# Kernel optimization log

Hardware: AMD Instinct MI355X
Metric: run time of the kernel (lower is better)

Reference implementation:

```python
import jax, jax.numpy as jnp
import numpy as np

L, D, H, N, B, R = 6, 1024, 16, 2048, 1, 10000
K = D // H
EPS = 1e-6


def setup_inputs() -> dict:
    key = jax.random.key(0)
    ks = jax.random.split(key, 7)
    s = 0.02
    return {
        "x": jax.random.normal(ks[0], (B, N, D), dtype=jnp.float32),
        "qkv_w": jax.random.normal(ks[1], (L, 3 * D, D), dtype=jnp.float32) * s,
        "out_w": jax.random.normal(ks[2], (L, D, D), dtype=jnp.float32) * s,
        "w1": jax.random.normal(ks[3], (L, 8 * D, D), dtype=jnp.float32) * s,
        "w2": jax.random.normal(ks[4], (L, D, 4 * D), dtype=jnp.float32) * s,
        "norm1_w": jnp.ones((L, D), dtype=jnp.float32),
        "norm2_w": jnp.ones((L, D), dtype=jnp.float32),
    }


def _rmsnorm(x, w):
    var = jnp.mean(jnp.square(x), axis=-1, keepdims=True)
    return x * jax.lax.rsqrt(var + EPS) * w


def _rope_tables():
    inv_freq = 1.0 / (R ** (jnp.arange(0, K, 2, dtype=jnp.float32) / K))
    t = jnp.arange(N, dtype=jnp.float32)
    freqs = jnp.outer(t, inv_freq)            # (N, K/2)
    emb = jnp.concatenate([freqs, freqs], -1)  # (N, K)
    # broadcast over (B, N, H, K)
    return jnp.cos(emb)[None, :, None, :], jnp.sin(emb)[None, :, None, :]


def _rotate_half(x):
    x1, x2 = jnp.split(x, 2, axis=-1)
    return jnp.concatenate([-x2, x1], axis=-1)


def _apply_rope(q, k, cos, sin):
    return q * cos + _rotate_half(q) * sin, k * cos + _rotate_half(k) * sin


def reference(x, qkv_w, out_w, w1, w2, norm1_w, norm2_w):
    cos, sin = _rope_tables()
    causal = jnp.tril(jnp.ones((N, N), dtype=bool))  # (N_query, M_key)
    scale = 1.0 / jnp.sqrt(jnp.float32(K))
    for i in range(L):
        # --- attention block (pre-norm) ---
        h = _rmsnorm(x, norm1_w[i])
        qkv = jnp.einsum('bnd,ed->bne', h, qkv_w[i]).reshape(B, N, 3, H, K)
        q, k, v = qkv[:, :, 0], qkv[:, :, 1], qkv[:, :, 2]
        q, k = _apply_rope(q, k, cos, sin)
        scores = jnp.einsum('bnhk,bmhk->bnhm', q, k) * scale
        scores = jnp.where(causal[None, :, None, :], scores, -jnp.inf)
        probs = jax.nn.softmax(scores, axis=-1)
        attn = jnp.einsum('bnhm,bmhk->bnhk', probs, v).reshape(B, N, D)
        x = x + jnp.einsum('bnd,ed->bne', attn, out_w[i])
        # --- SwiGLU MLP block (pre-norm) ---
        h = _rmsnorm(x, norm2_w[i])
        a = jnp.einsum('bnd,ed->bne', h, w1[i])  # (B, N, 8D)
        a1, a2 = jnp.split(a, 2, axis=-1)
        g = jax.nn.silu(a1) * a2                 # (B, N, 4D)
        x = x + jnp.einsum('bnf,df->bnd', g, w2[i])
    return x
```

## Files before the change

kernel.cpp:

```cpp
#include <hip/hip_runtime.h>
#include <math.h>

typedef short bf16x8 __attribute__((ext_vector_type(8)));
typedef float floatx4 __attribute__((ext_vector_type(4)));

__device__ __forceinline__ unsigned short f2bf(float f) {
    unsigned int u = __float_as_uint(f);
    u += 0x7fffu + ((u >> 16) & 1u);
    return (unsigned short)(u >> 16);
}
__device__ __forceinline__ float bf2f(unsigned short u) {
    return __uint_as_float(((unsigned int)u) << 16);
}
__device__ __forceinline__ void async16(void* lds, const void* g) {
    __builtin_amdgcn_global_load_lds((const __attribute__((address_space(1))) unsigned int*)g,
                                     (__attribute__((address_space(3))) unsigned int*)lds,
                                     16, 0, 0);
}

__global__ __launch_bounds__(256) void conv_w(
        const float* __restrict__ qkv, const float* __restrict__ ow,
        const float* __restrict__ w1, const float* __restrict__ w2,
        unsigned short* __restrict__ dst) {
    size_t i = (size_t)blockIdx.x * 256 + threadIdx.x;
    const float* s; size_t off; unsigned short* d;
    if (i < 786432)       { s = qkv; off = i;           d = dst; }
    else if (i < 1048576) { s = ow;  off = i - 786432;  d = dst + 3145728; }
    else if (i < 3145728) { s = w1;  off = i - 1048576; d = dst + 4194304; }
    else                  { s = w2;  off = i - 3145728; d = dst + 12582912; }
    float4 v = ((const float4*)s)[off];
    ushort4 o;
    o.x = f2bf(v.x); o.y = f2bf(v.y); o.z = f2bf(v.z); o.w = f2bf(v.w);
    ((ushort4*)d)[off] = o;
}

__global__ __launch_bounds__(256) void rmsnorm_bf(
        const float* __restrict__ x, const float* __restrict__ w,
        unsigned short* __restrict__ out) {
    __shared__ float sred[4];
    int row = blockIdx.x;
    int t = threadIdx.x;
    float4 v = ((const float4*)(x + (size_t)row * 1024))[t];
    float ss = v.x*v.x + v.y*v.y + v.z*v.z + v.w*v.w;
#pragma unroll
    for (int m = 32; m >= 1; m >>= 1) ss += __shfl_xor(ss, m, 64);
    if ((t & 63) == 0) sred[t >> 6] = ss;
    __syncthreads();
    float tot = sred[0] + sred[1] + sred[2] + sred[3];
    float r = rsqrtf(tot * (1.0f / 1024.0f) + 1e-6f);
    float4 wv = ((const float4*)w)[t];
    ushort4 o;
    o.x = f2bf(v.x * r * wv.x); o.y = f2bf(v.y * r * wv.y);
    o.z = f2bf(v.z * r * wv.z); o.w = f2bf(v.w * r * wv.w);
    ((ushort4*)(out + (size_t)row * 1024))[t] = o;
}

template<int OUTMODE>
__global__ __launch_bounds__(256) void gemm_bf(
        const unsigned short* __restrict__ A, const unsigned short* __restrict__ W,
        void* __restrict__ Cout, int Ncols, int Kd) {
    __shared__ __align__(16) unsigned short As[128 * 32];
    __shared__ __align__(16) unsigned short Bs[128 * 32];
    int t = threadIdx.x;
    int wave = t >> 6, lane = t & 63;
    int wm = wave >> 1, wn = wave & 1;
    int lrow = lane & 15, quad = lane >> 4;
    int bmBase = blockIdx.y * 128, bnBase = blockIdx.x * 128;
    int kslice = Kd / gridDim.z;
    int kBeg = blockIdx.z * kslice, kEnd = kBeg + kslice;

    int sub = lane >> 2;
    int colb = (lane & 3) * 8;
    int c0 = wave, c1 = wave + 4;

    floatx4 acc[4][4] = {};

    for (int k0 = kBeg; k0 < kEnd; k0 += 32) {
        async16(&As[c0 * 512 + lane * 8], A + (size_t)(bmBase + c0 * 16 + sub) * Kd + k0 + colb);
        async16(&As[c1 * 512 + lane * 8], A + (size_t)(bmBase + c1 * 16 + sub) * Kd + k0 + colb);
        async16(&Bs[c0 * 512 + lane * 8], W + (size_t)(bnBase + c0 * 16 + sub) * Kd + k0 + colb);
        async16(&Bs[c1 * 512 + lane * 8], W + (size_t)(bnBase + c1 * 16 + sub) * Kd + k0 + colb);
        __syncthreads();
        bf16x8 af[4], bfr[4];
#pragma unroll
        for (int im = 0; im < 4; im++)
            af[im] = *(const bf16x8*)&As[(wm * 64 + im * 16 + lrow) * 32 + quad * 8];
#pragma unroll
        for (int in = 0; in < 4; in++)
            bfr[in] = *(const bf16x8*)&Bs[(wn * 64 + in * 16 + lrow) * 32 + quad * 8];
#pragma unroll
        for (int im = 0; im < 4; im++)
#pragma unroll
            for (int in = 0; in < 4; in++)
                acc[im][in] = __builtin_amdgcn_mfma_f32_16x16x32_bf16(af[im], bfr[in], acc[im][in], 0, 0, 0);
        __syncthreads();
    }

#pragma unroll
    for (int im = 0; im < 4; im++) {
        int gr0 = bmBase + wm * 64 + im * 16 + quad * 4;
#pragma unroll
        for (int in = 0; in < 4; in++) {
            int gc = bnBase + wn * 64 + in * 16 + lrow;
#pragma unroll
            for (int r2 = 0; r2 < 4; r2++) {
                size_t off = (size_t)(gr0 + r2) * Ncols + gc;
                if (OUTMODE == 0) ((unsigned short*)Cout)[off] = f2bf(acc[im][in][r2]);
                else              atomicAdd((float*)Cout + off, acc[im][in][r2]);
            }
        }
    }
}

__global__ __launch_bounds__(512) void rope_bf(
        const unsigned short* __restrict__ qkv, unsigned short* __restrict__ q,
        unsigned short* __restrict__ k, unsigned short* __restrict__ vt) {
    int n = blockIdx.x;
    int t = threadIdx.x;
    int h = t >> 5, j = t & 31;
    float inv = powf(10000.0f, -(float)j * (1.0f / 32.0f));
    float ang = (float)n * inv;
    float s = sinf(ang), c = cosf(ang);
    const unsigned short* base = qkv + (size_t)n * 3072;
    int o1 = h * 64 + j, o2 = o1 + 32;
    float q1 = bf2f(base[o1]),        q2 = bf2f(base[o2]);
    float k1 = bf2f(base[1024 + o1]), k2 = bf2f(base[1024 + o2]);
    q[(size_t)n * 1024 + o1] = f2bf(q1 * c - q2 * s);
    q[(size_t)n * 1024 + o2] = f2bf(q2 * c + q1 * s);
    k[(size_t)n * 1024 + o1] = f2bf(k1 * c - k2 * s);
    k[(size_t)n * 1024 + o2] = f2bf(k2 * c + k1 * s);
    vt[(size_t)o1 * 2048 + n] = base[2048 + o1];
    vt[(size_t)o2 * 2048 + n] = base[2048 + o2];
}

__global__ __launch_bounds__(256) void attn_bf(
        const unsigned short* __restrict__ q, const unsigned short* __restrict__ kbuf,
        const unsigned short* __restrict__ vt, unsigned short* __restrict__ attn) {
    __shared__ __align__(16) unsigned short Qs[64 * 64];
    __shared__ __align__(16) unsigned short Ks[64 * 64];
    __shared__ __align__(16) unsigned short Vs[64 * 64];
    __shared__ __align__(16) unsigned short Ps[4 * 16 * 64];
    int qb = blockIdx.x;
    int h  = blockIdx.y;
    int t = threadIdx.x;
    int wave = t >> 6, lane = t & 63;
    int lrow = lane & 15, quad = lane >> 4;
    int sub8 = lane >> 3;
    int col8 = (lane & 7) * 8;
    int c0 = wave, c1 = wave + 4;

    async16(&Qs[c0 * 512 + lane * 8], q + (size_t)(qb * 64 + c0 * 8 + sub8) * 1024 + h * 64 + col8);
    async16(&Qs[c1 * 512 + lane * 8], q + (size_t)(qb * 64 + c1 * 8 + sub8) * 1024 + h * 64 + col8);

    floatx4 oacc[4] = {};
    float mrow[4], lsum[4];
#pragma unroll
    for (int r2 = 0; r2 < 4; r2++) { mrow[r2] = -INFINITY; lsum[r2] = 0.0f; }

    for (int kt = 0; kt <= qb; ++kt) {
        __syncthreads();
        async16(&Ks[c0 * 512 + lane * 8], kbuf + (size_t)(kt * 64 + c0 * 8 + sub8) * 1024 + h * 64 + col8);
        async16(&Ks[c1 * 512 + lane * 8], kbuf + (size_t)(kt * 64 + c1 * 8 + sub8) * 1024 + h * 64 + col8);
        async16(&Vs[c0 * 512 + lane * 8], vt + (size_t)(h * 64 + c0 * 8 + sub8) * 2048 + kt * 64 + col8);
        async16(&Vs[c1 * 512 + lane * 8], vt + (size_t)(h * 64 + c1 * 8 + sub8) * 2048 + kt * 64 + col8);
        __syncthreads();

        floatx4 sacc[4] = {};
#pragma unroll
        for (int kk = 0; kk < 64; kk += 32) {
            bf16x8 aq = *(const bf16x8*)&Qs[(wave * 16 + lrow) * 64 + kk + quad * 8];
#pragma unroll
            for (int jn = 0; jn < 4; jn++) {
                bf16x8 bk = *(const bf16x8*)&Ks[(jn * 16 + lrow) * 64 + kk + quad * 8];
                sacc[jn] = __builtin_amdgcn_mfma_f32_16x16x32_bf16(aq, bk, sacc[jn], 0, 0, 0);
            }
        }

#pragma unroll
        for (int r2 = 0; r2 < 4; r2++) {
            int qg = qb * 64 + wave * 16 + quad * 4 + r2;
            float sv[4];
            float rm = -INFINITY;
#pragma unroll
            for (int jn = 0; jn < 4; jn++) {
                float xv = sacc[jn][r2] * 0.125f;
                int kg = kt * 64 + jn * 16 + lrow;
                if (kg > qg) xv = -INFINITY;
                sv[jn] = xv;
                rm = fmaxf(rm, xv);
            }
#pragma unroll
            for (int m = 8; m >= 1; m >>= 1) rm = fmaxf(rm, __shfl_xor(rm, m, 64));
            float mnew = fmaxf(mrow[r2], rm);
            float alpha = __expf(mrow[r2] - mnew);
            float rs = 0.0f;
#pragma unroll
            for (int jn = 0; jn < 4; jn++) {
                float p = __expf(sv[jn] - mnew);
                rs += p;
                Ps[wave * 1024 + (quad * 4 + r2) * 64 + jn * 16 + lrow] = f2bf(p);
            }
#pragma unroll
            for (int m = 8; m >= 1; m >>= 1) rs += __shfl_xor(rs, m, 64);
            lsum[r2] = lsum[r2] * alpha + rs;
            mrow[r2] = mnew;
#pragma unroll
            for (int jd = 0; jd < 4; jd++) oacc[jd][r2] *= alpha;
        }
        __syncthreads();

#pragma unroll
        for (int kk = 0; kk < 64; kk += 32) {
            bf16x8 ap = *(const bf16x8*)&Ps[wave * 1024 + lrow * 64 + kk + quad * 8];
#pragma unroll
            for (int jd = 0; jd < 4; jd++) {
                bf16x8 bv = *(const bf16x8*)&Vs[(jd * 16 + lrow) * 64 + kk + quad * 8];
                oacc[jd] = __builtin_amdgcn_mfma_f32_16x16x32_bf16(ap, bv, oacc[jd], 0, 0, 0);
            }
        }
    }

#pragma unroll
    for (int r2 = 0; r2 < 4; r2++) {
        int qg = qb * 64 + wave * 16 + quad * 4 + r2;
        float invl = 1.0f / lsum[r2];
#pragma unroll
        for (int jd = 0; jd < 4; jd++)
            attn[(size_t)qg * 1024 + h * 64 + jd * 16 + lrow] = f2bf(oacc[jd][r2] * invl);
    }
}

__global__ __launch_bounds__(256) void silu_bf(
        const unsigned short* __restrict__ a, unsigned short* __restrict__ g) {
    int i = blockIdx.x * 256 + threadIdx.x;
    int n = i >> 10, c = (i & 1023) << 2;
    ushort4 a1 = *(const ushort4*)(a + (size_t)n * 8192 + c);
    ushort4 a2 = *(const ushort4*)(a + (size_t)n * 8192 + 4096 + c);
    float x0 = bf2f(a1.x), x1 = bf2f(a1.y), x2 = bf2f(a1.z), x3 = bf2f(a1.w);
    ushort4 o;
    o.x = f2bf(x0 / (1.0f + __expf(-x0)) * bf2f(a2.x));
    o.y = f2bf(x1 / (1.0f + __expf(-x1)) * bf2f(a2.y));
    o.z = f2bf(x2 / (1.0f + __expf(-x2)) * bf2f(a2.z));
    o.w = f2bf(x3 / (1.0f + __expf(-x3)) * bf2f(a2.w));
    *(ushort4*)(g + (size_t)n * 4096 + c) = o;
}

extern "C" void kernel_launch(void* const* d_in, const int* in_sizes, int n_in,
                              void* d_out, int out_size, void* d_ws, size_t ws_size,
                              hipStream_t stream) {
    const float* x     = (const float*)d_in[0];
    const float* qkv_w = (const float*)d_in[1];
    const float* out_w = (const float*)d_in[2];
    const float* w1    = (const float*)d_in[3];
    const float* w2    = (const float*)d_in[4];
    const float* n1    = (const float*)d_in[5];
    const float* n2    = (const float*)d_in[6];

    char* ws = (char*)d_ws;
    float*          xbuf  = (float*)ws;
    unsigned short* hbuf  = (unsigned short*)(ws + 8388608);
    unsigned short* wslot = (unsigned short*)(ws + 12582912);
    char*           arena = ws + 46137344;
    unsigned short* qkvb  = (unsigned short*)arena;
    unsigned short* qb_   = (unsigned short*)(arena + 12582912);
    unsigned short* kb_   = (unsigned short*)(arena + 16777216);
    unsigned short* vtb   = (unsigned short*)(arena + 20971520);
    unsigned short* attnb = (unsigned short*)(arena + 25165824);
    unsigned short* abuf  = (unsigned short*)arena;
    unsigned short* gbuf  = (unsigned short*)(arena + 33554432);

    unsigned short* qkvw_bf = wslot;
    unsigned short* outw_bf = wslot + 3145728;
    unsigned short* w1_bf   = wslot + 4194304;
    unsigned short* w2_bf   = wslot + 12582912;

    hipMemcpyAsync(xbuf, x, (size_t)2048 * 1024 * 4, hipMemcpyDeviceToDevice, stream);

    for (int i = 0; i < 6; i++) {
        conv_w<<<16384, 256, 0, stream>>>(qkv_w + (size_t)i * 3145728, out_w + (size_t)i * 1048576,
                                          w1 + (size_t)i * 8388608, w2 + (size_t)i * 4194304, wslot);
        rmsnorm_bf<<<2048, 256, 0, stream>>>(xbuf, n1 + (size_t)i * 1024, hbuf);
        gemm_bf<0><<<dim3(24, 16, 1), 256, 0, stream>>>(hbuf, qkvw_bf, qkvb, 3072, 1024);
        rope_bf<<<2048, 512, 0, stream>>>(qkvb, qb_, kb_, vtb);
        attn_bf<<<dim3(32, 16), 256, 0, stream>>>(qb_, kb_, vtb, attnb);
        gemm_bf<1><<<dim3(8, 16, 2), 256, 0, stream>>>(attnb, outw_bf, xbuf, 1024, 1024);
        rmsnorm_bf<<<2048, 256, 0, stream>>>(xbuf, n2 + (size_t)i * 1024, hbuf);
        gemm_bf<0><<<dim3(64, 16, 1), 256, 0, stream>>>(hbuf, w1_bf, abuf, 8192, 1024);
        silu_bf<<<8192, 256, 0, stream>>>(abuf, gbuf);
        gemm_bf<1><<<dim3(8, 16, 4), 256, 0, stream>>>(gbuf, w2_bf, xbuf, 1024, 4096);
    }

    hipMemcpyAsync(d_out, xbuf, (size_t)2048 * 1024 * 4, hipMemcpyDeviceToDevice, stream);
}
```

Measured before the change: 2.108 ms.

## Fuse RoPE into QKV GEMM, SiLU into W1 GEMM, batch weight conversion

The QKV GEMM epilogue now applies the rotary embedding directly and writes Q, K and transposed V, which removes the separate rope kernel and the intermediate qkv buffer. The W1 GEMM computes the gate and up tiles together and applies SiLU in its epilogue, so the 8D activation round-trip and the silu kernel go away. All six layers' weights are converted to bf16 in a single launch up front rather than once per layer. The trade-offs are higher register pressure in the dual-accumulator GEMM, half as many blocks for the W1 GEMM, and a larger workspace.

After: 3.470 ms. 64.6% more time.

```diff
diff --git a/kernel.cpp b/kernel.cpp
--- a/kernel.cpp
+++ b/kernel.cpp
@@ -18,20 +18,33 @@
                                      16, 0, 0);
 }
 
-__global__ __launch_bounds__(256) void conv_w(
+__global__ __launch_bounds__(256) void conv_all(
         const float* __restrict__ qkv, const float* __restrict__ ow,
         const float* __restrict__ w1, const float* __restrict__ w2,
         unsigned short* __restrict__ dst) {
     size_t i = (size_t)blockIdx.x * 256 + threadIdx.x;
-    const float* s; size_t off; unsigned short* d;
-    if (i < 786432)       { s = qkv; off = i;           d = dst; }
-    else if (i < 1048576) { s = ow;  off = i - 786432;  d = dst + 3145728; }
-    else if (i < 3145728) { s = w1;  off = i - 1048576; d = dst + 4194304; }
-    else                  { s = w2;  off = i - 3145728; d = dst + 12582912; }
-    float4 v = ((const float4*)s)[off];
+    const float4* s; size_t didx;
+    if (i < 4718592) {
+        size_t layer = i / 786432, off = i % 786432;
+        s = (const float4*)qkv + layer * 786432 + off;
+        didx = layer * 4194304 + off;
+    } else if (i < 6291456) {
+        size_t j = i - 4718592, layer = j / 262144, off = j % 262144;
+        s = (const float4*)ow + layer * 262144 + off;
+        didx = layer * 4194304 + 786432 + off;
+    } else if (i < 18874368) {
+        size_t j = i - 6291456, layer = j / 2097152, off = j % 2097152;
+        s = (const float4*)w1 + layer * 2097152 + off;
+        didx = layer * 4194304 + 1048576 + off;
+    } else {
+        size_t j = i - 18874368, layer = j / 1048576, off = j % 1048576;
+        s = (const float4*)w2 + layer * 1048576 + off;
+        didx = layer * 4194304 + 3145728 + off;
+    }
+    float4 v = *s;
     ushort4 o;
     o.x = f2bf(v.x); o.y = f2bf(v.y); o.z = f2bf(v.z); o.w = f2bf(v.w);
-    ((ushort4*)d)[off] = o;
+    ((ushort4*)dst)[didx] = o;
 }
 
 __global__ __launch_bounds__(256) void rmsnorm_bf(
@@ -55,10 +68,9 @@
     ((ushort4*)(out + (size_t)row * 1024))[t] = o;
 }
 
-template<int OUTMODE>
-__global__ __launch_bounds__(256) void gemm_bf(
+__global__ __launch_bounds__(256) void gemm_atomic(
         const unsigned short* __restrict__ A, const unsigned short* __restrict__ W,
-        void* __restrict__ Cout, int Ncols, int Kd) {
+        float* __restrict__ Cout, int Ncols, int Kd) {
     __shared__ __align__(16) unsigned short As[128 * 32];
     __shared__ __align__(16) unsigned short Bs[128 * 32];
     int t = threadIdx.x;
@@ -68,9 +80,7 @@
     int bmBase = blockIdx.y * 128, bnBase = blockIdx.x * 128;
     int kslice = Kd / gridDim.z;
     int kBeg = blockIdx.z * kslice, kEnd = kBeg + kslice;
-
-    int sub = lane >> 2;
-    int colb = (lane & 3) * 8;
+    int sub = lane >> 2, colb = (lane & 3) * 8;
     int c0 = wave, c1 = wave + 4;
 
     floatx4 acc[4][4] = {};
@@ -103,34 +113,148 @@
         for (int in = 0; in < 4; in++) {
             int gc = bnBase + wn * 64 + in * 16 + lrow;
 #pragma unroll
+            for (int r2 = 0; r2 < 4; r2++)
+                atomicAdd(Cout + (size_t)(gr0 + r2) * Ncols + gc, acc[im][in][r2]);
+        }
+    }
+}
+
+__global__ __launch_bounds__(256) void gemm_qkv(
+        const unsigned short* __restrict__ A, const unsigned short* __restrict__ W,
+        unsigned short* __restrict__ qout, unsigned short* __restrict__ kout,
+        unsigned short* __restrict__ vtout) {
+    __shared__ __align__(16) unsigned short As[128 * 32];
+    __shared__ __align__(16) unsigned short Bs[128 * 32];
+    const int Kd = 1024;
+    int t = threadIdx.x;
+    int wave = t >> 6, lane = t & 63;
+    int wm = wave >> 1, wn = wave & 1;
+    int lrow = lane & 15, quad = lane >> 4;
+    int bmBase = blockIdx.y * 128, bnBase = blockIdx.x * 128;
+    int sub = lane >> 2, colb = (lane & 3) * 8;
+    int c0 = wave, c1 = wave + 4;
+
+    floatx4 acc[4][4] = {};
+
+    for (int k0 = 0; k0 < Kd; k0 += 32) {
+        async16(&As[c0 * 512 + lane * 8], A + (size_t)(bmBase + c0 * 16 + sub) * Kd + k0 + colb);
+        async16(&As[c1 * 512 + lane * 8], A + (size_t)(bmBase + c1 * 16 + sub) * Kd + k0 + colb);
+        async16(&Bs[c0 * 512 + lane * 8], W + (size_t)(bnBase + c0 * 16 + sub) * Kd + k0 + colb);
+        async16(&Bs[c1 * 512 + lane * 8], W + (size_t)(bnBase + c1 * 16 + sub) * Kd + k0 + colb);
+        __syncthreads();
+        bf16x8 af[4], bfr[4];
+#pragma unroll
+        for (int im = 0; im < 4; im++)
+            af[im] = *(const bf16x8*)&As[(wm * 64 + im * 16 + lrow) * 32 + quad * 8];
+#pragma unroll
+        for (int in = 0; in < 4; in++)
+            bfr[in] = *(const bf16x8*)&Bs[(wn * 64 + in * 16 + lrow) * 32 + quad * 8];
+#pragma unroll
+        for (int im = 0; im < 4; im++)
+#pragma unroll
+            for (int in = 0; in < 4; in++)
+                acc[im][in] = __builtin_amdgcn_mfma_f32_16x16x32_bf16(af[im], bfr[in], acc[im][in], 0, 0, 0);
+        __syncthreads();
+    }
+
+    int region = bnBase >> 10;
+    int cb = bnBase & 1023;
+    int headbase = cb + wn * 64;
+    if (region < 2) {
+        unsigned short* dst = (region == 0) ? qout : kout;
+#pragma unroll
+        for (int in = 0; in < 2; in++) {
+            int j = in * 16 + lrow;
+            float invf = exp2f(-(float)j * (13.2877123795494f / 32.0f));
+#pragma unroll
+            for (int im = 0; im < 4; im++) {
+                int n0 = bmBase + wm * 64 + im * 16 + quad * 4;
+#pragma unroll
+                for (int r2 = 0; r2 < 4; r2++) {
+                    int n = n0 + r2;
+                    float ang = (float)n * invf;
+                    float s = sinf(ang), c = cosf(ang);
+                    float x1 = acc[im][in][r2], x2 = acc[im][in + 2][r2];
+                    dst[(size_t)n * 1024 + headbase + j]      = f2bf(x1 * c - x2 * s);
+                    dst[(size_t)n * 1024 + headbase + j + 32] = f2bf(x2 * c + x1 * s);
+                }
+            }
+        }
+    } else {
+#pragma unroll
+        for (int im = 0; im < 4; im++) {
+            int n0 = bmBase + wm * 64 + im * 16 + quad * 4;
+#pragma unroll
+            for (int in = 0; in < 4; in++) {
+                int d = headbase + in * 16 + lrow;
+                ushort4 o;
+                o.x = f2bf(acc[im][in][0]); o.y = f2bf(acc[im][in][1]);
+                o.z = f2bf(acc[im][in][2]); o.w = f2bf(acc[im][in][3]);
+                *(ushort4*)&vtout[(size_t)d * 2048 + n0] = o;
+            }
+        }
+    }
+}
+
+__global__ __launch_bounds__(256) void gemm_w1silu(
+        const unsigned short* __restrict__ A, const unsigned short* __restrict__ W,
+        unsigned short* __restrict__ g) {
+    __shared__ __align__(16) unsigned short As[128 * 32];
+    __shared__ __align__(16) unsigned short Bg[128 * 32];
+    __shared__ __align__(16) unsigned short Bu[128 * 32];
+    const int Kd = 1024;
+    int t = threadIdx.x;
+    int wave = t >> 6, lane = t & 63;
+    int wm = wave >> 1, wn = wave & 1;
+    int lrow = lane & 15, quad = lane >> 4;
+    int bmBase = blockIdx.y * 128, bnBase = blockIdx.x * 128;
+    int sub = lane >> 2, colb = (lane & 3) * 8;
+    int c0 = wave, c1 = wave + 4;
+
+    floatx4 accg[4][4] = {};
+    floatx4 accu[4][4] = {};
+
+    for (int k0 = 0; k0 < Kd; k0 += 32) {
+        async16(&As[c0 * 512 + lane * 8], A + (size_t)(bmBase + c0 * 16 + sub) * Kd + k0 + colb);
+        async16(&As[c1 * 512 + lane * 8], A + (size_t)(bmBase + c1 * 16 + sub) * Kd + k0 + colb);
+        async16(&Bg[c0 * 512 + lane * 8], W + (size_t)(bnBase + c0 * 16 + sub) * Kd + k0 + colb);
+        async16(&Bg[c1 * 512 + lane * 8], W + (size_t)(bnBase + c1 * 16 + sub) * Kd + k0 + colb);
+        async16(&Bu[c0 * 512 + lane * 8], W + (size_t)(4096 + bnBase + c0 * 16 + sub) * Kd + k0 + colb);
+        async16(&Bu[c1 * 512 + lane * 8], W + (size_t)(4096 + bnBase + c1 * 16 + sub) * Kd + k0 + colb);
+        __syncthreads();
+        bf16x8 af[4], bg[4], bu[4];
+#pragma unroll
+        for (int im = 0; im < 4; im++)
+            af[im] = *(const bf16x8*)&As[(wm * 64 + im * 16 + lrow) * 32 + quad * 8];
+#pragma unroll
+        for (int in = 0; in < 4; in++) {
+            bg[in] = *(const bf16x8*)&Bg[(wn * 64 + in * 16 + lrow) * 32 + quad * 8];
+            bu[in] = *(const bf16x8*)&Bu[(wn * 64 + in * 16 + lrow) * 32 + quad * 8];
+        }
+#pragma unroll
+        for (int im = 0; im < 4; im++)
+#pragma unroll
+            for (int in = 0; in < 4; in++) {
+                accg[im][in] = __builtin_amdgcn_mfma_f32_16x16x32_bf16(af[im], bg[in], accg[im][in], 0, 0, 0);
+                accu[im][in] = __builtin_amdgcn_mfma_f32_16x16x32_bf16(af[im], bu[in], accu[im][in], 0, 0, 0);
+            }
+        __syncthreads();
+    }
+
+#pragma unroll
+    for (int im = 0; im < 4; im++) {
+        int gr0 = bmBase + wm * 64 + im * 16 + quad * 4;
+#pragma unroll
+        for (int in = 0; in < 4; in++) {
+            int gc = bnBase + wn * 64 + in * 16 + lrow;
+#pragma unroll
             for (int r2 = 0; r2 < 4; r2++) {
-                size_t off = (size_t)(gr0 + r2) * Ncols + gc;
-                if (OUTMODE == 0) ((unsigned short*)Cout)[off] = f2bf(acc[im][in][r2]);
-                else              atomicAdd((float*)Cout + off, acc[im][in][r2]);
-            }
-        }
-    }
-}
-
-__global__ __launch_bounds__(512) void rope_bf(
-        const unsigned short* __restrict__ qkv, unsigned short* __restrict__ q,
-        unsigned short* __restrict__ k, unsigned short* __restrict__ vt) {
-    int n = blockIdx.x;
-    int t = threadIdx.x;
-    int h = t >> 5, j = t & 31;
-    float inv = powf(10000.0f, -(float)j * (1.0f / 32.0f));
-    float ang = (float)n * inv;
-    float s = sinf(ang), c = cosf(ang);
-    const unsigned short* base = qkv + (size_t)n * 3072;
-    int o1 = h * 64 + j, o2 = o1 + 32;
-    float q1 = bf2f(base[o1]),        q2 = bf2f(base[o2]);
-    float k1 = bf2f(base[1024 + o1]), k2 = bf2f(base[1024 + o2]);
-    q[(size_t)n * 1024 + o1] = f2bf(q1 * c - q2 * s);
-    q[(size_t)n * 1024 + o2] = f2bf(q2 * c + q1 * s);
-    k[(size_t)n * 1024 + o1] = f2bf(k1 * c - k2 * s);
-    k[(size_t)n * 1024 + o2] = f2bf(k2 * c + k1 * s);
-    vt[(size_t)o1 * 2048 + n] = base[2048 + o1];
-    vt[(size_t)o2 * 2048 + n] = base[2048 + o2];
+                float a1 = accg[im][in][r2], a2 = accu[im][in][r2];
+                float gv = a1 / (1.0f + __expf(-a1)) * a2;
+                g[(size_t)(gr0 + r2) * 4096 + gc] = f2bf(gv);
+            }
+        }
+    }
 }
 
 __global__ __launch_bounds__(256) void attn_bf(
@@ -145,8 +269,7 @@
     int t = threadIdx.x;
     int wave = t >> 6, lane = t & 63;
     int lrow = lane & 15, quad = lane >> 4;
-    int sub8 = lane >> 3;
-    int col8 = (lane & 7) * 8;
+    int sub8 = lane >> 3, col8 = (lane & 7) * 8;
     int c0 = wave, c1 = wave + 4;
 
     async16(&Qs[c0 * 512 + lane * 8], q + (size_t)(qb * 64 + c0 * 8 + sub8) * 1024 + h * 64 + col8);
@@ -228,21 +351,6 @@
         for (int jd = 0; jd < 4; jd++)
             attn[(size_t)qg * 1024 + h * 64 + jd * 16 + lrow] = f2bf(oacc[jd][r2] * invl);
     }
-}
-
-__global__ __launch_bounds__(256) void silu_bf(
-        const unsigned short* __restrict__ a, unsigned short* __restrict__ g) {
-    int i = blockIdx.x * 256 + threadIdx.x;
-    int n = i >> 10, c = (i & 1023) << 2;
-    ushort4 a1 = *(const ushort4*)(a + (size_t)n * 8192 + c);
-    ushort4 a2 = *(const ushort4*)(a + (size_t)n * 8192 + 4096 + c);
-    float x0 = bf2f(a1.x), x1 = bf2f(a1.y), x2 = bf2f(a1.z), x3 = bf2f(a1.w);
-    ushort4 o;
-    o.x = f2bf(x0 / (1.0f + __expf(-x0)) * bf2f(a2.x));
-    o.y = f2bf(x1 / (1.0f + __expf(-x1)) * bf2f(a2.y));
-    o.z = f2bf(x2 / (1.0f + __expf(-x2)) * bf2f(a2.z));
-    o.w = f2bf(x3 / (1.0f + __expf(-x3)) * bf2f(a2.w));
-    *(ushort4*)(g + (size_t)n * 4096 + c) = o;
 }
 
 extern "C" void kernel_launch(void* const* d_in, const int* in_sizes, int n_in,
@@ -259,35 +367,30 @@
     char* ws = (char*)d_ws;
     float*          xbuf  = (float*)ws;
     unsigned short* hbuf  = (unsigned short*)(ws + 8388608);
-    unsigned short* wslot = (unsigned short*)(ws + 12582912);
-    char*           arena = ws + 46137344;
-    unsigned short* qkvb  = (unsigned short*)arena;
-    unsigned short* qb_   = (unsigned short*)(arena + 12582912);
-    unsigned short* kb_   = (unsigned short*)(arena + 16777216);
-    unsigned short* vtb   = (unsigned short*)(arena + 20971520);
-    unsigned short* attnb = (unsigned short*)(arena + 25165824);
-    unsigned short* abuf  = (unsigned short*)arena;
-    unsigned short* gbuf  = (unsigned short*)(arena + 33554432);
-
-    unsigned short* qkvw_bf = wslot;
-    unsigned short* outw_bf = wslot + 3145728;
-    unsigned short* w1_bf   = wslot + 4194304;
-    unsigned short* w2_bf   = wslot + 12582912;
+    unsigned short* qb_   = (unsigned short*)(ws + 12582912);
+    unsigned short* kb_   = (unsigned short*)(ws + 16777216);
+    unsigned short* vtb   = (unsigned short*)(ws + 20971520);
+    unsigned short* attnb = (unsigned short*)(ws + 25165824);
+    unsigned short* gbuf  = (unsigned short*)(ws + 29360128);
+    unsigned short* wslot = (unsigned short*)(ws + 46137344);
 
     hipMemcpyAsync(xbuf, x, (size_t)2048 * 1024 * 4, hipMemcpyDeviceToDevice, stream);
+    conv_all<<<98304, 256, 0, stream>>>(qkv_w, out_w, w1, w2, wslot);
 
     for (int i = 0; i < 6; i++) {
-        conv_w<<<16384, 256, 0, stream>>>(qkv_w + (size_t)i * 3145728, out_w + (size_t)i * 1048576,
-                                          w1 + (size_t)i * 8388608, w2 + (size_t)i * 4194304, wslot);
+        unsigned short* wb = wslot + (size_t)i * 16777216;
+        unsigned short* qkvw = wb;
+        unsigned short* outw = wb + 3145728;
+        unsigned short* w1w  = wb + 4194304;
+        unsigned short* w2w  = wb + 12582912;
+
         rmsnorm_bf<<<2048, 256, 0, stream>>>(xbuf, n1 + (size_t)i * 1024, hbuf);
-        gemm_bf<0><<<dim3(24, 16, 1), 256, 0, stream>>>(hbuf, qkvw_bf, qkvb, 3072, 1024);
-        rope_bf<<<2048, 512, 0, stream>>>(qkvb, qb_, kb_, vtb);
+        gemm_qkv<<<dim3(24, 16), 256, 0, stream>>>(hbuf, qkvw, qb_, kb_, vtb);
         attn_bf<<<dim3(32, 16), 256, 0, stream>>>(qb_, kb_, vtb, attnb);
-        gemm_bf<1><<<dim3(8, 16, 2), 256, 0, stream>>>(attnb, outw_bf, xbuf, 1024, 1024);
+        gemm_atomic<<<dim3(8, 16, 2), 256, 0, stream>>>(attnb, outw, xbuf, 1024, 1024);
         rmsnorm_bf<<<2048, 256, 0, stream>>>(xbuf, n2 + (size_t)i * 1024, hbuf);
-        gemm_bf<0><<<dim3(64, 16, 1), 256, 0, stream>>>(hbuf, w1_bf, abuf, 8192, 1024);
-        silu_bf<<<8192, 256, 0, stream>>>(abuf, gbuf);
-        gemm_bf<1><<<dim3(8, 16, 4), 256, 0, stream>>>(gbuf, w2_bf, xbuf, 1024, 4096);
+        gemm_w1silu<<<dim3(32, 16), 256, 0, stream>>>(hbuf, w1w, gbuf);
+        gemm_atomic<<<dim3(8, 16, 4), 256, 0, stream>>>(gbuf, w2w, xbuf, 1024, 4096);
     }
 
     hipMemcpyAsync(d_out, xbuf, (size_t)2048 * 1024 * 4, hipMemcpyDeviceToDevice, stream);
```
